# Kernel tuning notes

Measured on AMD Instinct MI355X. Metric: run time of the kernel, lower is better.

The kernel has to match this reference:

```python
import jax, jax.numpy as jnp
import numpy as np
import math

B, T, D, H = 4, 2048, 1024, 16
DH = D // H

def setup_inputs() -> dict:
    key = jax.random.key(0)
    ks = jax.random.split(key, 5)
    scale = 1.0 / math.sqrt(D)
    x = jax.random.normal(ks[0], (B, T, D), dtype=jnp.float32)
    Wq = jax.random.normal(ks[1], (D, D), dtype=jnp.float32) * scale
    Wk = jax.random.normal(ks[2], (D, D), dtype=jnp.float32) * scale
    Wv = jax.random.normal(ks[3], (D, D), dtype=jnp.float32) * scale
    Wo = jax.random.normal(ks[4], (D, D), dtype=jnp.float32) * scale
    mask = jnp.tril(jnp.ones((T, T), dtype=jnp.int32))  # causal, 1=keep
    return {"x": x, "mask": mask, "Wq": Wq, "Wk": Wk, "Wv": Wv, "Wo": Wo}

def reference(x, mask, Wq, Wk, Wv, Wo):
    Bx, Tx, Dx = x.shape
    # nn.Linear(bias=False): y = x @ W.T
    q = (x @ Wq.T).reshape(Bx, Tx, H, DH).transpose(0, 2, 1, 3)  # [B,H,T,dh]
    k = (x @ Wk.T).reshape(Bx, Tx, H, DH).transpose(0, 2, 1, 3)
    v = (x @ Wv.T).reshape(Bx, Tx, H, DH).transpose(0, 2, 1, 3)
    scores = jnp.einsum('bhqd,bhkd->bhqk', q, k) / math.sqrt(DH)
    m = mask[None, None, :, :]  # [1,1,T,T]
    scores = scores + (m == 0).astype(scores.dtype) * -1e9
    attn = jax.nn.softmax(scores, axis=-1)  # stable (max-subtract) like original
    out = jnp.einsum('bhqk,bhkd->bhqd', attn, v)
    out = out.transpose(0, 2, 1, 3).reshape(Bx, Tx, Dx)
    return out @ Wo.T
```

## Files before the change

### kernel.cpp

```cpp
#include <hip/hip_runtime.h>
#include <stdint.h>

#define B_  4
#define T_  2048
#define D_  1024
#define H_  16
#define DH_ 64

typedef unsigned short u16;
typedef __attribute__((ext_vector_type(8))) short bf16x8;
typedef __attribute__((ext_vector_type(8))) unsigned short u16x8;
typedef __attribute__((ext_vector_type(4))) unsigned short u16x4;
typedef __attribute__((ext_vector_type(4))) float f32x4;

#define NT_ ((size_t)B_ * T_ * D_)
#define QSCALE 0.18033688011112043f

__device__ __forceinline__ u16 f2bf(float f) {
    union { float f; uint32_t u; } v; v.f = f;
    uint32_t r = v.u + 0x7FFFu + ((v.u >> 16) & 1u);
    return (u16)(r >> 16);
}

__device__ __forceinline__ uint32_t pack2(float lo, float hi) {
    union { float f; uint32_t u; } a, b; a.f = lo; b.f = hi;
    return __builtin_amdgcn_perm(b.u, a.u, 0x07060302u);
}

__device__ __forceinline__ void gl2lds16(const u16* g, u16* l) {
    __builtin_amdgcn_global_load_lds(
        (const __attribute__((address_space(1))) unsigned int*)g,
        (__attribute__((address_space(3))) unsigned int*)l,
        16, 0, 0);
}

#define VMCNT(n) asm volatile("s_waitcnt vmcnt(" #n ")" ::: "memory")
#define SB0()    __builtin_amdgcn_sched_barrier(0)

__device__ __forceinline__ bf16x8 ldsrd(const u16* base, int row, int ks,
                                        int lq, int swzr) {
    int off = row * 128 + ks * 64 + lq * 16;
    return *(const bf16x8*)((const char*)base + (off ^ swzr));
}

__global__ __launch_bounds__(256) void cvt_x_kernel(
    const float* __restrict__ src, u16* __restrict__ dst, int n8)
{
    int i = blockIdx.x * 256 + threadIdx.x;
    if (i >= n8) return;
    f32x4 a = ((const f32x4*)src)[2 * i];
    f32x4 b = ((const f32x4*)src)[2 * i + 1];
    u16x8 o;
    o[0]=f2bf(a[0]); o[1]=f2bf(a[1]); o[2]=f2bf(a[2]); o[3]=f2bf(a[3]);
    o[4]=f2bf(b[0]); o[5]=f2bf(b[1]); o[6]=f2bf(b[2]); o[7]=f2bf(b[3]);
    ((u16x8*)dst)[i] = o;
}

__global__ __launch_bounds__(256) void cvt_w_kernel(
    const float* __restrict__ w0, const float* __restrict__ w1,
    const float* __restrict__ w2, const float* __restrict__ w3,
    u16* __restrict__ dst)
{
    const float* src = (blockIdx.y == 0) ? w0 : (blockIdx.y == 1) ? w1
                     : (blockIdx.y == 2) ? w2 : w3;
    u16* d = dst + (size_t)blockIdx.y * (D_ * D_);
    int i = blockIdx.x * 256 + threadIdx.x;
    f32x4 a = ((const f32x4*)src)[2 * i];
    f32x4 b = ((const f32x4*)src)[2 * i + 1];
    u16x8 o;
    o[0]=f2bf(a[0]); o[1]=f2bf(a[1]); o[2]=f2bf(a[2]); o[3]=f2bf(a[3]);
    o[4]=f2bf(b[0]); o[5]=f2bf(b[1]); o[6]=f2bf(b[2]); o[7]=f2bf(b[3]);
    ((u16x8*)d)[i] = o;
}

template<int OUT_MODE>
__global__ __launch_bounds__(512) void gemm8_kernel(
    const u16* __restrict__ X, const u16* __restrict__ W,
    void* __restrict__ C, int M, int N, int K)
{
    __shared__ __align__(16) u16 Ab2[2][256 * 64];
    __shared__ __align__(16) u16 Bb2[2][192 * 64];

    const int tid  = threadIdx.x;
    const int wave = tid >> 6;
    const int lane = tid & 63;
    const int lq = lane >> 4, lm = lane & 15;
    const int wm = wave >> 2;
    const int wn = wave & 3;

    const int xcd = (int)blockIdx.x & 7;
    const int idx = (int)blockIdx.x >> 3;
    const int m0 = (((xcd & 3) << 3) + (idx & 7)) << 8;
    const int n0 = (((xcd >> 2) << 3) + (idx >> 3)) * 192;

    const int srow = wave * 8 + (lane >> 3);
    const int scol = ((lane & 7) ^ (lane >> 3)) << 3;
    const u16* gA = X + (size_t)(m0 + srow) * K + scol;
    const u16* gB = W + (size_t)(n0 + srow) * K + scol;
    const size_t rK64 = (size_t)64 * K;

    const int swzr = (lm & 7) << 4;

    f32x4 acc[8][3] = {};
    bf16x8 afA[2][2], afB[2][2];
    bf16x8 bqA[3][2], bqB[3][2];
    const int NT = K >> 6;

    gl2lds16(gA,            (u16*)Ab2[0] + wave * 512);
    gl2lds16(gA + rK64,     (u16*)Ab2[0] + 4096  + wave * 512);
    gl2lds16(gA + 2 * rK64, (u16*)Ab2[0] + 8192  + wave * 512);
    gl2lds16(gA + 3 * rK64, (u16*)Ab2[0] + 12288 + wave * 512);
    gl2lds16(gB,            (u16*)Bb2[0] + wave * 512);
    gl2lds16(gB + rK64,     (u16*)Bb2[0] + 4096  + wave * 512);
    gl2lds16(gB + 2 * rK64, (u16*)Bb2[0] + 8192  + wave * 512);
    gl2lds16(gB + 64,            (u16*)Bb2[1] + wave * 512);
    gl2lds16(gB + 64 + rK64,     (u16*)Bb2[1] + 4096  + wave * 512);
    gl2lds16(gB + 64 + 2 * rK64, (u16*)Bb2[1] + 8192  + wave * 512);
    VMCNT(3);
    __builtin_amdgcn_s_barrier();
#pragma unroll
    for (int i2 = 0; i2 < 2; ++i2)
#pragma unroll
        for (int ks = 0; ks < 2; ++ks)
            afA[i2][ks] = ldsrd(Ab2[0], wm * 128 + i2 * 16 + lm, ks, lq, swzr);
#pragma unroll
    for (int j = 0; j < 3; ++j)
#pragma unroll
        for (int ks = 0; ks < 2; ++ks)
            bqA[j][ks] = ldsrd(Bb2[0], wn * 48 + j * 16 + lm, ks, lq, swzr);

    auto tile_body = [&](int t, bf16x8 (&bqU)[3][2], bf16x8 (&bqF)[3][2])
        __attribute__((always_inline)) -> void {
        const u16* Ac = Ab2[t & 1];
        const u16* An = Ab2[(t + 1) & 1];
        const u16* Bn = Bb2[(t + 1) & 1];
        u16* Abn = (u16*)Ab2[(t + 1) & 1];
        u16* Bbc = (u16*)Bb2[t & 1];
        const bool stA = (t + 1 < NT);
        const bool stB = (t + 2 < NT);
        const u16* gAs = gA + (size_t)(t + 1) * 64;
        const u16* gBs = gB + (size_t)(t + 2) * 64;

#define MFMA_PH(Q, AF, BQ)                                                  \
        __builtin_amdgcn_s_setprio(1);                                      \
        _Pragma("unroll")                                                   \
        for (int ks = 0; ks < 2; ++ks)                                      \
            _Pragma("unroll")                                               \
            for (int i2 = 0; i2 < 2; ++i2)                                  \
                _Pragma("unroll")                                           \
                for (int j = 0; j < 3; ++j)                                 \
                    acc[2 * (Q) + i2][j] =                                  \
                        __builtin_amdgcn_mfma_f32_16x16x32_bf16(            \
                            AF[i2][ks], BQ[j][ks], acc[2 * (Q) + i2][j],    \
                            0, 0, 0);                                       \
        __builtin_amdgcn_s_setprio(0);

#define RD_AF(SET, P, BASE)                                                 \
        _Pragma("unroll")                                                   \
        for (int i2 = 0; i2 < 2; ++i2)                                      \
            _Pragma("unroll")                                               \
            for (int ks = 0; ks < 2; ++ks)                                  \
                SET[i2][ks] = ldsrd(BASE,                                   \
                    wm * 128 + (2 * (P) + i2) * 16 + lm, ks, lq, swzr);

        RD_AF(afB, 1, Ac);
        if (stA) {
            gl2lds16(gAs,        Abn + wave * 512);
            gl2lds16(gAs + rK64, Abn + 4096 + wave * 512);
        }
        SB0(); __builtin_amdgcn_s_barrier(); SB0();
        MFMA_PH(0, afA, bqU); SB0();
        __builtin_amdgcn_s_barrier();

        RD_AF(afA, 2, Ac);
        if (stA) {
            gl2lds16(gAs + 2 * rK64, Abn + 8192  + wave * 512);
            gl2lds16(gAs + 3 * rK64, Abn + 12288 + wave * 512);
        }
        SB0(); __builtin_amdgcn_s_barrier(); SB0();
        MFMA_PH(1, afB, bqU); SB0();
        __builtin_amdgcn_s_barrier();

        RD_AF(afB, 3, Ac);
        if (stB) {
            gl2lds16(gBs,        Bbc + wave * 512);
            gl2lds16(gBs + rK64, Bbc + 4096 + wave * 512);
        }
        SB0(); __builtin_amdgcn_s_barrier(); SB0();
        MFMA_PH(2, afA, bqU); SB0();
        if (stB)      { VMCNT(2); }
        else if (stA) { VMCNT(0); }
        __builtin_amdgcn_s_barrier();

        if (stA) {
            RD_AF(afA, 0, An);
#pragma unroll
            for (int j = 0; j < 3; ++j)
#pragma unroll
                for (int ks = 0; ks < 2; ++ks)
                    bqF[j][ks] = ldsrd(Bn, wn * 48 + j * 16 + lm, ks, lq, swzr);
        }
        if (stB)
            gl2lds16(gBs + 2 * rK64, Bbc + 8192 + wave * 512);
        SB0(); __builtin_amdgcn_s_barrier(); SB0();
        MFMA_PH(3, afB, bqU); SB0();
        __builtin_amdgcn_s_barrier();
#undef RD_AF
#undef MFMA_PH
    };

#pragma unroll 1
    for (int tt = 0; tt < NT; tt += 2) {
        tile_body(tt,     bqA, bqB);
        tile_body(tt + 1, bqB, bqA);
    }

#pragma unroll
    for (int i = 0; i < 8; ++i)
#pragma unroll
        for (int j = 0; j < 3; ++j) {
            int rowb = m0 + wm * 128 + i * 16 + lq * 4;
            int col  = n0 + wn * 48 + j * 16 + lm;
            if (OUT_MODE == 2) {
#pragma unroll
                for (int r = 0; r < 4; ++r)
                    ((float*)C)[(size_t)(rowb + r) * N + col] = acc[i][j][r];
            } else {
                u16* Qp = (u16*)C;
                int region = col >> 10;
                int colr = col & 1023;
                if (region == 0) {
#pragma unroll
                    for (int r = 0; r < 4; ++r)
                        Qp[(size_t)(rowb + r) * D_ + colr] = f2bf(acc[i][j][r] * QSCALE);
                } else if (region == 1) {
#pragma unroll
                    for (int r = 0; r < 4; ++r)
                        (Qp + NT_)[(size_t)(rowb + r) * D_ + colr] = f2bf(acc[i][j][r]);
                } else {
                    int b = rowb >> 11, tt2 = rowb & (T_ - 1);
                    u16x4 pk;
#pragma unroll
                    for (int r = 0; r < 4; ++r) pk[r] = f2bf(acc[i][j][r]);
                    *(u16x4*)((Qp + 2 * NT_) + ((size_t)b * D_ + colr) * T_ + tt2) = pk;
                }
            }
        }
}

__global__ __launch_bounds__(512) void gemm8o_kernel(
    const u16* __restrict__ X, const u16* __restrict__ W,
    float* __restrict__ C)
{
    __shared__ __align__(16) u16 Ab2[2][256 * 64];
    __shared__ __align__(16) u16 Bb2[2][128 * 64];

    const int K = 1024, N = 1024;
    const int tid  = threadIdx.x;
    const int wave = tid >> 6;
    const int lane = tid & 63;
    const int lq = lane >> 4, lm = lane & 15;
    const int wm = wave >> 2;
    const int wn = wave & 3;

    const int xcd = (int)blockIdx.x & 7;
    const int idx = (int)blockIdx.x >> 3;
    const int m0 = (((xcd & 3) << 3) + (idx & 7)) << 8;
    const int n0 = (((xcd >> 2) << 2) + (idx >> 3)) << 7;

    const int srow = wave * 8 + (lane >> 3);
    const int scol = ((lane & 7) ^ (lane >> 3)) << 3;
    const u16* gA = X + (size_t)(m0 + srow) * K + scol;
    const u16* gB = W + (size_t)(n0 + srow) * K + scol;
    const size_t rK64 = (size_t)64 * K;

    const int swzr = (lm & 7) << 4;

    f32x4 acc[8][2] = {};
    bf16x8 afA[2][2], afB[2][2];
    bf16x8 bqA[2][2], bqB[2][2];
    const int NT = 16;

    gl2lds16(gA,            (u16*)Ab2[0] + wave * 512);
    gl2lds16(gA + rK64,     (u16*)Ab2[0] + 4096  + wave * 512);
    gl2lds16(gA + 2 * rK64, (u16*)Ab2[0] + 8192  + wave * 512);
    gl2lds16(gA + 3 * rK64, (u16*)Ab2[0] + 12288 + wave * 512);
    gl2lds16(gB,            (u16*)Bb2[0] + wave * 512);
    gl2lds16(gB + rK64,     (u16*)Bb2[0] + 4096  + wave * 512);
    gl2lds16(gB + 64,            (u16*)Bb2[1] + wave * 512);
    gl2lds16(gB + 64 + rK64,     (u16*)Bb2[1] + 4096  + wave * 512);
    VMCNT(2);
    __builtin_amdgcn_s_barrier();
#pragma unroll
    for (int i2 = 0; i2 < 2; ++i2)
#pragma unroll
        for (int ks = 0; ks < 2; ++ks)
            afA[i2][ks] = ldsrd(Ab2[0], wm * 128 + i2 * 16 + lm, ks, lq, swzr);
#pragma unroll
    for (int j = 0; j < 2; ++j)
#pragma unroll
        for (int ks = 0; ks < 2; ++ks)
            bqA[j][ks] = ldsrd(Bb2[0], wn * 32 + j * 16 + lm, ks, lq, swzr);

    auto tile_body = [&](int t, bf16x8 (&bqU)[2][2], bf16x8 (&bqF)[2][2])
        __attribute__((always_inline)) -> void {
        const u16* Ac = Ab2[t & 1];
        const u16* An = Ab2[(t + 1) & 1];
        const u16* Bn = Bb2[(t + 1) & 1];
        u16* Abn = (u16*)Ab2[(t + 1) & 1];
        u16* Bbc = (u16*)Bb2[t & 1];
        const bool stA = (t + 1 < NT);
        const bool stB = (t + 2 < NT);
        const u16* gAs = gA + (size_t)(t + 1) * 64;
        const u16* gBs = gB + (size_t)(t + 2) * 64;

#define MFMA_PHO(Q, AF, BQ)                                                 \
        __builtin_amdgcn_s_setprio(1);                                      \
        _Pragma("unroll")                                                   \
        for (int ks = 0; ks < 2; ++ks)                                      \
            _Pragma("unroll")                                               \
            for (int i2 = 0; i2 < 2; ++i2)                                  \
                _Pragma("unroll")                                           \
                for (int j = 0; j < 2; ++j)                                 \
                    acc[2 * (Q) + i2][j] =                                  \
                        __builtin_amdgcn_mfma_f32_16x16x32_bf16(            \
                            AF[i2][ks], BQ[j][ks], acc[2 * (Q) + i2][j],    \
                            0, 0, 0);                                       \
        __builtin_amdgcn_s_setprio(0);

#define RD_AFO(SET, P, BASE)                                                \
        _Pragma("unroll")                                                   \
        for (int i2 = 0; i2 < 2; ++i2)                                      \
            _Pragma("unroll")                                               \
            for (int ks = 0; ks < 2; ++ks)                                  \
                SET[i2][ks] = ldsrd(BASE,                                   \
                    wm * 128 + (2 * (P) + i2) * 16 + lm, ks, lq, swzr);

        RD_AFO(afB, 1, Ac);
        if (stA) {
            gl2lds16(gAs,        Abn + wave * 512);
            gl2lds16(gAs + rK64, Abn + 4096 + wave * 512);
        }
        SB0(); __builtin_amdgcn_s_barrier(); SB0();
        MFMA_PHO(0, afA, bqU); SB0();
        __builtin_amdgcn_s_barrier();

        RD_AFO(afA, 2, Ac);
        if (stA) {
            gl2lds16(gAs + 2 * rK64, Abn + 8192  + wave * 512);
            gl2lds16(gAs + 3 * rK64, Abn + 12288 + wave * 512);
        }
        SB0(); __builtin_amdgcn_s_barrier(); SB0();
        MFMA_PHO(1, afB, bqU); SB0();
        __builtin_amdgcn_s_barrier();

        RD_AFO(afB, 3, Ac);
        if (stB)
            gl2lds16(gBs, Bbc + wave * 512);
        SB0(); __builtin_amdgcn_s_barrier(); SB0();
        MFMA_PHO(2, afA, bqU); SB0();
        if (stB)      { VMCNT(1); }
        else if (stA) { VMCNT(0); }
        __builtin_amdgcn_s_barrier();

        if (stA) {
            RD_AFO(afA, 0, An);
#pragma unroll
            for (int j = 0; j < 2; ++j)
#pragma unroll
                for (int ks = 0; ks < 2; ++ks)
                    bqF[j][ks] = ldsrd(Bn, wn * 32 + j * 16 + lm, ks, lq, swzr);
        }
        if (stB)
            gl2lds16(gBs + rK64, Bbc + 4096 + wave * 512);
        SB0(); __builtin_amdgcn_s_barrier(); SB0();
        MFMA_PHO(3, afB, bqU); SB0();
        __builtin_amdgcn_s_barrier();
#undef RD_AFO
#undef MFMA_PHO
    };

#pragma unroll 1
    for (int tt = 0; tt < NT; tt += 2) {
        tile_body(tt,     bqA, bqB);
        tile_body(tt + 1, bqB, bqA);
    }

#pragma unroll
    for (int i = 0; i < 8; ++i)
#pragma unroll
        for (int j = 0; j < 2; ++j) {
            int rowb = m0 + wm * 128 + i * 16 + lq * 4;
            int col  = n0 + wn * 32 + j * 16 + lm;
#pragma unroll
            for (int r = 0; r < 4; ++r)
                C[(size_t)(rowb + r) * N + col] = acc[i][j][r];
        }
}

__global__ __launch_bounds__(128) void attn_kernel(
    const u16* __restrict__ Qg, const u16* __restrict__ Kg,
    const u16* __restrict__ Vtg, u16* __restrict__ Og)
{
    __shared__ __align__(16) u16 Pl[2 * 64 * 40];

    const int tid  = threadIdx.x;
    const int wave = tid >> 6;
    const int lane = tid & 63;
    const int lq = lane >> 4, lm = lane & 15;
    const int id = blockIdx.x;
    const int xs = id & 7;
    const int bh = xs + 8 * ((id >> 3) & 7);
    const int qj = 31 - (id >> 6);
    const int b = bh >> 4, h = bh & 15;

    const size_t batchoff = (size_t)b * T_ * D_;
    const size_t headoff  = (size_t)h * DH_;
    const size_t vbase    = (size_t)bh * DH_ * T_;

    u16* pw = Pl + wave * 64 * 40;

    const int qw  = qj * 64;
    const int ktd = qj >> 1;
    const int odd = qj & 1;

    bf16x8 aq[4][2];
#pragma unroll
    for (int qf = 0; qf < 4; ++qf) {
        const u16* qrow = Qg + batchoff + (size_t)(qw + qf * 16 + lm) * D_ + headoff;
        aq[qf][0] = *(const bf16x8*)(qrow + lq * 8);
        aq[qf][1] = *(const bf16x8*)(qrow + 32 + lq * 8);
    }

    f32x4 oaccT[4][4] = {};
    float l_lane[4] = {0.f, 0.f, 0.f, 0.f};

#pragma unroll 1
    for (int kt = wave; kt <= ktd; kt += 2) {
        const bool diag = (kt == ktd);
        const int ksmax = diag ? (odd ? 3 : 1) : 3;

#pragma unroll
        for (int c = 0; c < 4; ++c) {
            if (c <= ksmax) {
#pragma unroll
                for (int t = 0; t < 2; ++t) {
                    const int mt = 2 * c + t;
                    const u16* krow = Kg + batchoff
                        + (size_t)(kt * 128 + mt * 16 + lm) * D_ + headoff;
                    bf16x8 kf0 = *(const bf16x8*)(krow + lq * 8);
                    bf16x8 kf1 = *(const bf16x8*)(krow + 32 + lq * 8);
                    f32x4 s[4];
                    __builtin_amdgcn_s_setprio(1);
#pragma unroll
                    for (int qf = 0; qf < 4; ++qf) {
                        s[qf] = f32x4{0.f, 0.f, 0.f, 0.f};
                        s[qf] = __builtin_amdgcn_mfma_f32_16x16x32_bf16(
                            kf0, aq[qf][0], s[qf], 0, 0, 0);
                        s[qf] = __builtin_amdgcn_mfma_f32_16x16x32_bf16(
                            kf1, aq[qf][1], s[qf], 0, 0, 0);
                    }
                    __builtin_amdgcn_s_setprio(0);
                    if (diag) {
                        int keyb = kt * 128 + mt * 16 + lq * 4;
#pragma unroll
                        for (int qf = 0; qf < 4; ++qf) {
                            int query = qw + qf * 16 + lm;
#pragma unroll
                            for (int r = 0; r < 4; ++r)
                                if (keyb + r > query) s[qf][r] = -1e9f;
                        }
                    }
#pragma unroll
                    for (int qf = 0; qf < 4; ++qf) {
                        float p0 = __builtin_amdgcn_exp2f(s[qf][0]);
                        float p1 = __builtin_amdgcn_exp2f(s[qf][1]);
                        float p2 = __builtin_amdgcn_exp2f(s[qf][2]);
                        float p3 = __builtin_amdgcn_exp2f(s[qf][3]);
                        l_lane[qf] += (p0 + p1) + (p2 + p3);
                        uint2 d; d.x = pack2(p0, p1); d.y = pack2(p2, p3);
                        *(uint2*)(pw + (qf * 16 + lm) * 40 + t * 16 + lq * 4) = d;
                    }
                }

                bf16x8 pf[4];
#pragma unroll
                for (int qf = 0; qf < 4; ++qf)
                    pf[qf] = *(const bf16x8*)(pw + (qf * 16 + lm) * 40 + lq * 8);
                __builtin_amdgcn_s_setprio(1);
#pragma unroll
                for (int mo = 0; mo < 4; ++mo) {
                    const u16* vrow = Vtg + vbase
                        + (size_t)(mo * 16 + lm) * T_ + kt * 128 + c * 32;
                    bf16x8 vf = *(const bf16x8*)(vrow + lq * 8);
#pragma unroll
                    for (int qf = 0; qf < 4; ++qf)
                        oaccT[qf][mo] = __builtin_amdgcn_mfma_f32_16x16x32_bf16(
                            vf, pf[qf], oaccT[qf][mo], 0, 0, 0);
                }
                __builtin_amdgcn_s_setprio(0);
            }
        }
    }

    float* Cf = (float*)Pl;
    const int cswz = (lane ^ (lane >> 3)) * 4;
    __syncthreads();
    if (wave == 1) {
#pragma unroll
        for (int qf = 0; qf < 2; ++qf)
#pragma unroll
            for (int mo = 0; mo < 4; ++mo)
                *(f32x4*)&Cf[(qf * 4 + mo) * 256 + cswz] = oaccT[qf][mo];
#pragma unroll
        for (int qf = 0; qf < 4; ++qf)
            Cf[2048 + qf * 64 + lane] = l_lane[qf];
    }
    __syncthreads();
    if (wave == 0) {
#pragma unroll
        for (int qf = 0; qf < 2; ++qf)
#pragma unroll
            for (int mo = 0; mo < 4; ++mo) {
                f32x4 o = *(const f32x4*)&Cf[(qf * 4 + mo) * 256 + cswz];
#pragma unroll
                for (int r = 0; r < 4; ++r) oaccT[qf][mo][r] += o[r];
            }
#pragma unroll
        for (int qf = 0; qf < 4; ++qf) l_lane[qf] += Cf[2048 + qf * 64 + lane];
    }
    __syncthreads();
    if (wave == 1) {
#pragma unroll
        for (int qf = 2; qf < 4; ++qf)
#pragma unroll
            for (int mo = 0; mo < 4; ++mo)
                *(f32x4*)&Cf[((qf - 2) * 4 + mo) * 256 + cswz] = oaccT[qf][mo];
    }
    __syncthreads();
    if (wave == 0) {
#pragma unroll
        for (int qf = 2; qf < 4; ++qf)
#pragma unroll
            for (int mo = 0; mo < 4; ++mo) {
                f32x4 o = *(const f32x4*)&Cf[((qf - 2) * 4 + mo) * 256 + cswz];
#pragma unroll
                for (int r = 0; r < 4; ++r) oaccT[qf][mo][r] += o[r];
            }
#pragma unroll
        for (int qf = 0; qf < 4; ++qf) {
            float l = l_lane[qf];
            l += __shfl_xor(l, 16, 64);
            l += __shfl_xor(l, 32, 64);
            float inv = 1.0f / l;
            int row = qw + qf * 16 + lm;
            u16* obase = Og + batchoff + (size_t)row * D_ + headoff;
#pragma unroll
            for (int mo = 0; mo < 4; ++mo) {
                uint2 d;
                d.x = pack2(oaccT[qf][mo][0] * inv, oaccT[qf][mo][1] * inv);
                d.y = pack2(oaccT[qf][mo][2] * inv, oaccT[qf][mo][3] * inv);
                *(uint2*)(obase + mo * 16 + lq * 4) = d;
            }
        }
    }
}

extern "C" void kernel_launch(void* const* d_in, const int* in_sizes, int n_in,
                              void* d_out, int out_size, void* d_ws, size_t ws_size,
                              hipStream_t stream)
{
    const float* x  = (const float*)d_in[0];
    const float* Wq = (const float*)d_in[2];
    const float* Wk = (const float*)d_in[3];
    const float* Wv = (const float*)d_in[4];
    const float* Wo = (const float*)d_in[5];

    const size_t DD = (size_t)D_ * D_;
    u16* Qb  = (u16*)d_ws;
    u16* Kb  = Qb + NT_;
    u16* Vb  = Kb + NT_;
    u16* Ob  = Vb + NT_;
    u16* xb  = Ob + NT_;
    u16* wb  = xb + NT_;

    const int M = B_ * T_;

    cvt_x_kernel<<<dim3((int)(NT_ / 8 / 256)), 256, 0, stream>>>(x, xb, (int)(NT_ / 8));
    cvt_w_kernel<<<dim3((int)(DD / 8 / 256), 4), 256, 0, stream>>>(Wq, Wk, Wv, Wo, wb);

    gemm8_kernel<3><<<dim3((M / 256) * (3 * D_ / 192)), 512, 0, stream>>>(
        xb, wb, Qb, M, 3 * D_, D_);

    attn_kernel<<<dim3(2048), 128, 0, stream>>>(Qb, Kb, Vb, Ob);

    gemm8o_kernel<<<dim3(256), 512, 0, stream>>>(Ob, wb + 3 * DD, (float*)d_out);
}
```

Before: 269.3 us.

## Restructure GEMM main loop into two half-tile MFMA phases with explicit LDS waits

Replaces the four-phase, register double-buffered fragment pipeline (with cross-tile prefetch of A/B fragments) with a simpler per-tile loop. Each tile now does two phases: load four A fragments plus all B fragments, wait on lgkmcnt, run 24 MFMAs, then repeat for the second half. This cuts the number of barriers per tile and makes each MFMA burst larger. In exchange it drops the overlap between LDS reads for the next tile and the current MFMAs, and adds full lgkmcnt(0) stalls before each phase. All three B global loads are now issued in the second phase.

```diff
diff --git a/kernel.cpp b/kernel.cpp
--- a/kernel.cpp
+++ b/kernel.cpp
@@ -35,6 +35,7 @@
 }
 
 #define VMCNT(n) asm volatile("s_waitcnt vmcnt(" #n ")" ::: "memory")
+#define LGKM0()  asm volatile("s_waitcnt lgkmcnt(0)" ::: "memory")
 #define SB0()    __builtin_amdgcn_sched_barrier(0)
 
 __device__ __forceinline__ bf16x8 ldsrd(const u16* base, int row, int ks,
@@ -102,8 +103,6 @@
     const int swzr = (lm & 7) << 4;
 
     f32x4 acc[8][3] = {};
-    bf16x8 afA[2][2], afB[2][2];
-    bf16x8 bqA[3][2], bqB[3][2];
     const int NT = K >> 6;
 
     gl2lds16(gA,            (u16*)Ab2[0] + wave * 512);
@@ -118,22 +117,25 @@
     gl2lds16(gB + 64 + 2 * rK64, (u16*)Bb2[1] + 8192  + wave * 512);
     VMCNT(3);
     __builtin_amdgcn_s_barrier();
-#pragma unroll
-    for (int i2 = 0; i2 < 2; ++i2)
-#pragma unroll
-        for (int ks = 0; ks < 2; ++ks)
-            afA[i2][ks] = ldsrd(Ab2[0], wm * 128 + i2 * 16 + lm, ks, lq, swzr);
-#pragma unroll
-    for (int j = 0; j < 3; ++j)
-#pragma unroll
-        for (int ks = 0; ks < 2; ++ks)
-            bqA[j][ks] = ldsrd(Bb2[0], wn * 48 + j * 16 + lm, ks, lq, swzr);
-
-    auto tile_body = [&](int t, bf16x8 (&bqU)[3][2], bf16x8 (&bqF)[3][2])
-        __attribute__((always_inline)) -> void {
+
+#define MFMA_HALF(IOFF)                                                     \
+        __builtin_amdgcn_s_setprio(1);                                      \
+        _Pragma("unroll")                                                   \
+        for (int ks = 0; ks < 2; ++ks)                                      \
+            _Pragma("unroll")                                               \
+            for (int i4 = 0; i4 < 4; ++i4)                                  \
+                _Pragma("unroll")                                           \
+                for (int j = 0; j < 3; ++j)                                 \
+                    acc[(IOFF) + i4][j] =                                   \
+                        __builtin_amdgcn_mfma_f32_16x16x32_bf16(            \
+                            af[i4][ks], bq[j][ks], acc[(IOFF) + i4][j],     \
+                            0, 0, 0);                                       \
+        __builtin_amdgcn_s_setprio(0);
+
+#pragma unroll 1
+    for (int t = 0; t < NT; ++t) {
         const u16* Ac = Ab2[t & 1];
-        const u16* An = Ab2[(t + 1) & 1];
-        const u16* Bn = Bb2[(t + 1) & 1];
+        const u16* Bc = Bb2[t & 1];
         u16* Abn = (u16*)Ab2[(t + 1) & 1];
         u16* Bbc = (u16*)Bb2[t & 1];
         const bool stA = (t + 1 < NT);
@@ -141,79 +143,50 @@
         const u16* gAs = gA + (size_t)(t + 1) * 64;
         const u16* gBs = gB + (size_t)(t + 2) * 64;
 
-#define MFMA_PH(Q, AF, BQ)                                                  \
-        __builtin_amdgcn_s_setprio(1);                                      \
-        _Pragma("unroll")                                                   \
-        for (int ks = 0; ks < 2; ++ks)                                      \
-            _Pragma("unroll")                                               \
-            for (int i2 = 0; i2 < 2; ++i2)                                  \
-                _Pragma("unroll")                                           \
-                for (int j = 0; j < 3; ++j)                                 \
-                    acc[2 * (Q) + i2][j] =                                  \
-                        __builtin_amdgcn_mfma_f32_16x16x32_bf16(            \
-                            AF[i2][ks], BQ[j][ks], acc[2 * (Q) + i2][j],    \
-                            0, 0, 0);                                       \
-        __builtin_amdgcn_s_setprio(0);
-
-#define RD_AF(SET, P, BASE)                                                 \
-        _Pragma("unroll")                                                   \
-        for (int i2 = 0; i2 < 2; ++i2)                                      \
-            _Pragma("unroll")                                               \
-            for (int ks = 0; ks < 2; ++ks)                                  \
-                SET[i2][ks] = ldsrd(BASE,                                   \
-                    wm * 128 + (2 * (P) + i2) * 16 + lm, ks, lq, swzr);
-
-        RD_AF(afB, 1, Ac);
+        bf16x8 af[4][2], bq[3][2];
+
+#pragma unroll
+        for (int i4 = 0; i4 < 4; ++i4)
+#pragma unroll
+            for (int ks = 0; ks < 2; ++ks)
+                af[i4][ks] = ldsrd(Ac, wm * 128 + i4 * 16 + lm, ks, lq, swzr);
+#pragma unroll
+        for (int j = 0; j < 3; ++j)
+#pragma unroll
+            for (int ks = 0; ks < 2; ++ks)
+                bq[j][ks] = ldsrd(Bc, wn * 48 + j * 16 + lm, ks, lq, swzr);
         if (stA) {
             gl2lds16(gAs,        Abn + wave * 512);
             gl2lds16(gAs + rK64, Abn + 4096 + wave * 512);
         }
-        SB0(); __builtin_amdgcn_s_barrier(); SB0();
-        MFMA_PH(0, afA, bqU); SB0();
-        __builtin_amdgcn_s_barrier();
-
-        RD_AF(afA, 2, Ac);
+        SB0(); __builtin_amdgcn_s_barrier();
+        LGKM0(); SB0();
+        MFMA_HALF(0)
+        SB0(); __builtin_amdgcn_s_barrier();
+
+#pragma unroll
+        for (int i4 = 0; i4 < 4; ++i4)
+#pragma unroll
+            for (int ks = 0; ks < 2; ++ks)
+                af[i4][ks] = ldsrd(Ac, wm * 128 + (4 + i4) * 16 + lm, ks, lq, swzr);
         if (stA) {
             gl2lds16(gAs + 2 * rK64, Abn + 8192  + wave * 512);
             gl2lds16(gAs + 3 * rK64, Abn + 12288 + wave * 512);
         }
-        SB0(); __builtin_amdgcn_s_barrier(); SB0();
-        MFMA_PH(1, afB, bqU); SB0();
-        __builtin_amdgcn_s_barrier();
-
-        RD_AF(afB, 3, Ac);
         if (stB) {
-            gl2lds16(gBs,        Bbc + wave * 512);
-            gl2lds16(gBs + rK64, Bbc + 4096 + wave * 512);
-        }
-        SB0(); __builtin_amdgcn_s_barrier(); SB0();
-        MFMA_PH(2, afA, bqU); SB0();
-        if (stB)      { VMCNT(2); }
+            gl2lds16(gBs,            Bbc + wave * 512);
+            gl2lds16(gBs + rK64,     Bbc + 4096 + wave * 512);
+            gl2lds16(gBs + 2 * rK64, Bbc + 8192 + wave * 512);
+        }
+        SB0(); __builtin_amdgcn_s_barrier();
+        LGKM0(); SB0();
+        MFMA_HALF(4)
+        SB0();
+        if (stB)      { VMCNT(3); }
         else if (stA) { VMCNT(0); }
         __builtin_amdgcn_s_barrier();
-
-        if (stA) {
-            RD_AF(afA, 0, An);
-#pragma unroll
-            for (int j = 0; j < 3; ++j)
-#pragma unroll
-                for (int ks = 0; ks < 2; ++ks)
-                    bqF[j][ks] = ldsrd(Bn, wn * 48 + j * 16 + lm, ks, lq, swzr);
-        }
-        if (stB)
-            gl2lds16(gBs + 2 * rK64, Bbc + 8192 + wave * 512);
-        SB0(); __builtin_amdgcn_s_barrier(); SB0();
-        MFMA_PH(3, afB, bqU); SB0();
-        __builtin_amdgcn_s_barrier();
-#undef RD_AF
-#undef MFMA_PH
-    };
-
-#pragma unroll 1
-    for (int tt = 0; tt < NT; tt += 2) {
-        tile_body(tt,     bqA, bqB);
-        tile_body(tt + 1, bqB, bqA);
-    }
+    }
+#undef MFMA_HALF
 
 #pragma unroll
     for (int i = 0; i < 8; ++i)
```

After: 268.8 us. Within noise of the previous version (-0.2%).
